# Kernel optimization log

Hardware: AMD Instinct MI355X
Metric: run time of the kernel (lower is better)

Reference implementation:

```python
import jax, jax.numpy as jnp
import numpy as np

K = 5          # number of neighbors (self excluded)
EPS = 1e-7     # distance epsilon
Q = 0.98       # quantile for radius normalization


def _cdist(A):
    # Euclidean pairwise distances [N, N] via the matmul expansion.
    sq = jnp.sum(A * A, axis=-1)
    d2 = sq[:, None] + sq[None, :] - 2.0 * (A @ A.T)
    return jnp.sqrt(jnp.maximum(d2, 0.0))


def _lid(values):
    # values: [N, K] ascending neighbor distances; LID via log-distance ratios.
    norm = values[:, -1:]
    return -jnp.sum(jnp.log10(values) - jnp.log10(norm), axis=1)


def setup_inputs() -> dict:
    key = jax.random.key(0)
    k1, k2 = jax.random.split(key)
    X = jax.random.normal(k1, (8192, 256), dtype=jnp.float32)
    Z = jax.random.normal(k2, (8192, 64), dtype=jnp.float32)
    return {"X": X, "Z": Z}


def reference(X, Z):
    n = X.shape[0]
    normA1 = jnp.quantile(jnp.linalg.norm(X - jnp.mean(X, axis=0), axis=1), Q)
    normA2 = jnp.quantile(jnp.linalg.norm(Z - jnp.mean(Z, axis=0), axis=1), Q)

    # k-NN in X space (drop self at column 0)
    x_dist = (_cdist(X) + EPS) / normA1
    neg_vals, idx = jax.lax.top_k(-x_dist, K + 1)   # smallest K+1, ascending
    values = (-neg_vals)[:, 1:]
    nn_mask = idx[:, 1:]
    lid_X = _lid(values)

    # gather the SAME neighbor indices in Z space
    z_dist = (_cdist(Z) + EPS) / normA2
    extracted = jnp.take_along_axis(z_dist, nn_mask, axis=1)
    lid_Z = _lid(extracted)

    return jnp.sum(jnp.square(lid_X - lid_Z)) / (n * K * 10)
```

## Files before the change

### kernel.cpp

```cpp
#include <hip/hip_runtime.h>
#include <math.h>
#include <stdint.h>

#define EPS     1e-7f
#define NR      8192
#define DX      256
#define DZ      64
#define KNN     5
#define KEEP    6
#define NSPLIT  8
#define NPOOL   (NSPLIT * KEEP)
#define NCAND   16
#define JS      (NR / NSPLIT)
#define JT      64
#define NCHUNK  (JS / JT)
#define RBLK    64
#define SC1     0x7F7F7F7F

typedef float f32x4 __attribute__((ext_vector_type(4)));
typedef int   i32x8 __attribute__((ext_vector_type(8)));

__device__ __forceinline__ uint32_t umin_(uint32_t a, uint32_t b) { return a < b ? a : b; }
__device__ __forceinline__ uint32_t umax_(uint32_t a, uint32_t b) { return a < b ? b : a; }

__device__ __forceinline__ uint32_t to_e4m3(float f) {
    const uint32_t u = __float_as_uint(f);
    const uint32_t s = (u >> 24) & 0x80u;
    const int e = (int)((u >> 23) & 0xFFu) - 127;
    if (e < -10) return s;
    if (e > 8)   return s | 0x7Eu;
    const uint32_t mant = (u & 0x7FFFFFu) | 0x800000u;
    const int shift = (e < -6) ? (14 - e) : 20;
    uint32_t q = (mant + (1u << (shift - 1))) >> shift;
    int E = (e < -6) ? 0 : (e + 7);
    if (q >= 16) { q >>= 1; E += 1; }
    if (E == 0) return s | q;
    return s | ((uint32_t)E << 3) | (q & 7u);
}

__global__ __launch_bounds__(256) void split_k(const float* __restrict__ X,
                                               uint8_t* __restrict__ Xq,
                                               float* __restrict__ sqX,
                                               float* __restrict__ out) {
    if (blockIdx.x == 0 && threadIdx.x == 0) out[0] = 0.0f;
    const int row  = blockIdx.x * 4 + (threadIdx.x >> 6);
    const int lane = threadIdx.x & 63;
    const float4 v = *(const float4*)&X[(size_t)row * DX + lane * 4];
    float s = v.x * v.x + v.y * v.y + v.z * v.z + v.w * v.w;
    const uint32_t b = to_e4m3(v.x) | (to_e4m3(v.y) << 8) |
                       (to_e4m3(v.z) << 16) | (to_e4m3(v.w) << 24);
    ((uint32_t*)Xq)[(size_t)row * (DX / 4) + lane] = b;
    #pragma unroll
    for (int o = 32; o > 0; o >>= 1) s += __shfl_down(s, o);
    if (lane == 0) sqX[row] = s;
}

__global__ __launch_bounds__(256, 2) void mfma_topk_k(const uint8_t* __restrict__ Xq,
                                                      const float* __restrict__ sqX,
                                                      uint32_t* __restrict__ partials) {
    __shared__ __align__(16) uint8_t smem[16384];
    __shared__ uint32_t mb2[RBLK][2][KNN];
    const uint4* Bv = (const uint4*)smem;

    const int tid  = threadIdx.x;
    const int w    = tid >> 6;
    const int lane = tid & 63;
    const int n    = lane & 15;
    const int quad = lane >> 4;
    const int x7   = n & 7;
    const int h    = w >> 1;
    const int sp   = w & 1;
    const int s    = blockIdx.x & 7;
    const int ib   = (blockIdx.x >> 3) * RBLK;
    const int jb0  = s * JS;
    const int rowbase = ib + h * 32;

    i32x8 Aq[2][2];
    #pragma unroll
    for (int g = 0; g < 2; ++g)
        #pragma unroll
        for (int kf = 0; kf < 2; ++kf)
            Aq[g][kf] = *(const i32x8*)(Xq + (size_t)(rowbase + g * 16 + n) * DX
                                        + kf * 128 + quad * 32);

    float sqi[2][4];
    #pragma unroll
    for (int g = 0; g < 2; ++g) {
        const float4 t = *(const float4*)&sqX[rowbase + g * 16 + quad * 4];
        sqi[g][0] = t.x; sqi[g][1] = t.y; sqi[g][2] = t.z; sqi[g][3] = t.w;
    }

    uint32_t best[8][KNN];
    #pragma unroll
    for (int q = 0; q < 8; ++q)
        #pragma unroll
        for (int k = 0; k < KNN; ++k) best[q][k] = 0xFFFFFFFFu;

    int srcoff[4];
    #pragma unroll
    for (int u = 0; u < 4; ++u) {
        const int q  = w * 256 + u * 64 + lane;
        const int sj = q >> 4;
        const int c  = (q & 15) ^ (sj & 7);
        srcoff[u] = sj * DX + c * 16;
    }

    for (int jc = 0; jc < NCHUNK; ++jc) {
        const int jb = jb0 + jc * JT;
        __syncthreads();
        #pragma unroll
        for (int u = 0; u < 4; ++u) {
            const uint8_t* src = Xq + (size_t)jb * DX + srcoff[u];
            uint8_t* dst = smem + (size_t)(w * 256 + u * 64) * 16;
            __builtin_amdgcn_global_load_lds((const __attribute__((address_space(1))) uint32_t*)src,
                                             (__attribute__((address_space(3))) uint32_t*)dst,
                                             16, 0, 0);
        }
        __syncthreads();

        f32x4 acc[2][2];
        #pragma unroll
        for (int si = 0; si < 2; ++si)
            #pragma unroll
            for (int g = 0; g < 2; ++g)
                #pragma unroll
                for (int r = 0; r < 4; ++r) acc[si][g][r] = 0.0f;

        #pragma unroll
        for (int kf = 0; kf < 2; ++kf) {
            #pragma unroll
            for (int si = 0; si < 2; ++si) {
                const int sj = (sp * 2 + si) * 16 + n;
                const int cb = kf * 8 + quad * 2;
                const uint4 p0 = Bv[sj * 16 + (cb ^ x7)];
                const uint4 p1 = Bv[sj * 16 + ((cb + 1) ^ x7)];
                i32x8 b;
                b[0] = p0.x; b[1] = p0.y; b[2] = p0.z; b[3] = p0.w;
                b[4] = p1.x; b[5] = p1.y; b[6] = p1.z; b[7] = p1.w;
                acc[si][0] = __builtin_amdgcn_mfma_scale_f32_16x16x128_f8f6f4(
                                 Aq[0][kf], b, acc[si][0], 0, 0, 0, SC1, 0, SC1);
                acc[si][1] = __builtin_amdgcn_mfma_scale_f32_16x16x128_f8f6f4(
                                 Aq[1][kf], b, acc[si][1], 0, 0, 0, SC1, 0, SC1);
            }
        }

        #pragma unroll
        for (int si = 0; si < 2; ++si) {
            const int j = jb + (sp * 2 + si) * 16 + n;
            const float sqj = sqX[j];
            #pragma unroll
            for (int g = 0; g < 2; ++g) {
                #pragma unroll
                for (int r = 0; r < 4; ++r) {
                    const int i = rowbase + g * 16 + quad * 4 + r;
                    const float d2 = fmaf(-2.0f, acc[si][g][r], sqi[g][r] + sqj);
                    uint32_t cand = (__float_as_uint(d2) & 0xFFFFE000u) | (uint32_t)j;
                    cand = (j == i) ? 0xFFFFFFFFu : cand;
                    const int q = g * 4 + r;
                    if (cand < best[q][KNN - 1]) {
                        uint32_t ck = cand;
                        #pragma unroll
                        for (int k = 0; k < KNN; ++k) {
                            const uint32_t bk = best[q][k];
                            best[q][k] = umin_(ck, bk); ck = umax_(ck, bk);
                        }
                    }
                }
            }
        }
    }

    #pragma unroll
    for (int q = 0; q < 8; ++q) {
        uint32_t a0 = best[q][0], a1 = best[q][1], a2 = best[q][2],
                 a3 = best[q][3], a4 = best[q][4];
        #pragma unroll
        for (int mask = 1; mask <= 8; mask <<= 1) {
            const uint32_t b0 = __shfl_xor(a0, mask);
            const uint32_t b1 = __shfl_xor(a1, mask);
            const uint32_t b2 = __shfl_xor(a2, mask);
            const uint32_t b3 = __shfl_xor(a3, mask);
            const uint32_t b4 = __shfl_xor(a4, mask);
            const uint32_t c0 = umin_(a0, b0);
            const uint32_t c1 = umin_(umin_(a1, b1), umax_(a0, b0));
            const uint32_t c2 = umin_(umin_(a2, b2), umin_(umax_(a0, b1), umax_(a1, b0)));
            const uint32_t c3 = umin_(umin_(a3, b3),
                                      umin_(umax_(a1, b1), umin_(umax_(a0, b2), umax_(a2, b0))));
            const uint32_t c4 = umin_(umin_(a4, b4),
                                      umin_(umin_(umax_(a0, b3), umax_(a1, b2)),
                                            umin_(umax_(a2, b1), umax_(a3, b0))));
            a0 = c0; a1 = c1; a2 = c2; a3 = c3; a4 = c4;
        }
        const int rloc = h * 32 + (q >> 2) * 16 + quad * 4 + (q & 3);
        uint32_t v = a0;
        v = (n == 1) ? a1 : v;
        v = (n == 2) ? a2 : v;
        v = (n == 3) ? a3 : v;
        v = (n == 4) ? a4 : v;
        if (n < KNN) mb2[rloc][sp][n] = v;
    }
    __syncthreads();

    if (tid < RBLK) {
        const uint32_t a0 = mb2[tid][0][0], a1 = mb2[tid][0][1], a2 = mb2[tid][0][2],
                       a3 = mb2[tid][0][3], a4 = mb2[tid][0][4];
        const uint32_t b0 = mb2[tid][1][0], b1 = mb2[tid][1][1], b2 = mb2[tid][1][2],
                       b3 = mb2[tid][1][3], b4 = mb2[tid][1][4];
        uint32_t o[KEEP];
        o[0] = umin_(a0, b0);
        o[1] = umin_(umin_(a1, b1), umax_(a0, b0));
        o[2] = umin_(umin_(a2, b2), umin_(umax_(a0, b1), umax_(a1, b0)));
        o[3] = umin_(umin_(a3, b3), umin_(umax_(a1, b1), umin_(umax_(a0, b2), umax_(a2, b0))));
        o[4] = umin_(umin_(a4, b4), umin_(umin_(umax_(a0, b3), umax_(a1, b2)),
                                          umin_(umax_(a2, b1), umax_(a3, b0))));
        o[5] = umin_(umin_(umax_(a0, b4), umax_(a4, b0)),
                     umin_(umax_(a1, b3), umin_(umax_(a2, b2), umax_(a3, b1))));
        #pragma unroll
        for (int k = 0; k < KEEP; ++k)
            partials[(size_t)(ib + tid) * NPOOL + s * KEEP + k] = o[k];
    }
}

__global__ __launch_bounds__(256) void finalize_k(const uint32_t* __restrict__ parts,
                                                  const float* __restrict__ X,
                                                  const float* __restrict__ Z,
                                                  const float* __restrict__ sqX,
                                                  float* __restrict__ out) {
    __shared__ float wsum[4];
    const int wv   = threadIdx.x >> 6;
    const int lane = threadIdx.x & 63;
    const int i    = blockIdx.x * 4 + wv;

    uint32_t v = (lane < NPOOL) ? parts[(size_t)i * NPOOL + lane] : 0xFFFFFFFFu;
    #pragma unroll
    for (int kk = 2; kk <= 64; kk <<= 1) {
        #pragma unroll
        for (int jj = kk >> 1; jj > 0; jj >>= 1) {
            const uint32_t o = __shfl_xor(v, jj);
            const bool keepmin = ((lane & kk) == 0) == ((lane & jj) == 0);
            v = keepmin ? umin_(v, o) : umax_(v, o);
        }
    }

    const float4 xi = *(const float4*)(X + (size_t)i * DX + lane * 4);

    float p[16];
    #pragma unroll
    for (int c = 0; c < NCAND; ++c) {
        const int jc = (int)(__shfl(v, c) & 0x1FFFu);
        const float4 xj = *(const float4*)(X + (size_t)jc * DX + lane * 4);
        p[c] = fmaf(xi.x, xj.x, fmaf(xi.y, xj.y, fmaf(xi.z, xj.z, xi.w * xj.w)));
    }
    #pragma unroll
    for (int c = 0; c < NCAND; ++c) {
        p[c] += __shfl_xor(p[c], 1);
        p[c] += __shfl_xor(p[c], 2);
        p[c] += __shfl_xor(p[c], 4);
        p[c] += __shfl_xor(p[c], 8);
    }
    const int cs = lane & 15;
    float dotv = p[0];
    dotv = (cs == 1)  ? p[1]  : dotv;
    dotv = (cs == 2)  ? p[2]  : dotv;
    dotv = (cs == 3)  ? p[3]  : dotv;
    dotv = (cs == 4)  ? p[4]  : dotv;
    dotv = (cs == 5)  ? p[5]  : dotv;
    dotv = (cs == 6)  ? p[6]  : dotv;
    dotv = (cs == 7)  ? p[7]  : dotv;
    dotv = (cs == 8)  ? p[8]  : dotv;
    dotv = (cs == 9)  ? p[9]  : dotv;
    dotv = (cs == 10) ? p[10] : dotv;
    dotv = (cs == 11) ? p[11] : dotv;
    dotv = (cs == 12) ? p[12] : dotv;
    dotv = (cs == 13) ? p[13] : dotv;
    dotv = (cs == 14) ? p[14] : dotv;
    dotv = (cs == 15) ? p[15] : dotv;
    dotv += __shfl_xor(dotv, 16);
    dotv += __shfl_xor(dotv, 32);

    unsigned long long k16 = 0xFFFFFFFFFFFFFFFFull;
    const int jl = (int)(v & 0x1FFFu);
    if (lane < NCAND) {
        const float d2x = (sqX[i] + sqX[jl]) - 2.0f * dotv;
        k16 = ((unsigned long long)__float_as_uint(d2x) << 32) | (unsigned)jl;
    }
    #pragma unroll
    for (int kk = 2; kk <= 16; kk <<= 1) {
        #pragma unroll
        for (int jj = kk >> 1; jj > 0; jj >>= 1) {
            const unsigned long long o = __shfl_xor(k16, jj);
            const bool keepmin = ((lane & kk) == 0) == ((lane & jj) == 0);
            k16 = keepmin ? (k16 < o ? k16 : o) : (k16 < o ? o : k16);
        }
    }

    const float d2k = __uint_as_float((uint32_t)(k16 >> 32));
    const int   jk  = (int)(k16 & 0x1FFFull);
    float lkx = 0.0f;
    if (lane < KNN) lkx = log10f(sqrtf(fmaxf(d2k, 0.0f)) + EPS);
    const float l4x = __shfl(lkx, KNN - 1);
    float sx = lkx;
    sx += __shfl_xor(sx, 1);
    sx += __shfl_xor(sx, 2);
    sx += __shfl_xor(sx, 4);

    const float zi = Z[(size_t)i * DZ + lane];
    float zsum = 0.0f, l4z = 0.0f;
    #pragma unroll
    for (int k = 0; k < KNN; ++k) {
        const int jz = __shfl(jk, k);
        const float zj = Z[(size_t)jz * DZ + lane];
        const float d = zi - zj;
        float s = d * d;
        s += __shfl_xor(s, 1);
        s += __shfl_xor(s, 2);
        s += __shfl_xor(s, 4);
        s += __shfl_xor(s, 8);
        s += __shfl_xor(s, 16);
        s += __shfl_xor(s, 32);
        const float lk = log10f(sqrtf(fmaxf(s, 0.0f)) + EPS);
        zsum += lk;
        if (k == KNN - 1) l4z = lk;
    }

    if (lane == 0) {
        const float lx = -(__shfl(sx, 0) - (float)KNN * l4x);
        const float lz = -(zsum - (float)KNN * l4z);
        const float diff = lx - lz;
        wsum[wv] = diff * diff * (1.0f / ((float)NR * KNN * 10.0f));
    }
    __syncthreads();
    if (threadIdx.x == 0)
        atomicAdd(out, wsum[0] + wsum[1] + wsum[2] + wsum[3]);
}

extern "C" void kernel_launch(void* const* d_in, const int* in_sizes, int n_in,
                              void* d_out, int out_size, void* d_ws, size_t ws_size,
                              hipStream_t stream) {
    const float* X = (const float*)d_in[0];
    const float* Z = (const float*)d_in[1];
    float* out = (float*)d_out;

    char* ws = (char*)d_ws;
    float*     sqX      = (float*)ws;
    uint32_t*  partials = (uint32_t*)(ws + 32768);
    uint8_t*   Xq       = (uint8_t*)(ws + 32768 + 2097152);

    split_k<<<NR / 4, 256, 0, stream>>>(X, Xq, sqX, out);
    mfma_topk_k<<<(NR / RBLK) * NSPLIT, 256, 0, stream>>>(Xq, sqX, partials);
    finalize_k<<<NR / 4, 256, 0, stream>>>(partials, X, Z, sqX, out);
}
```

Baseline: 156.5 us.

## Fold norm term into MFMA accumulator init and merge candidate pairs branchlessly

The top-k epilogue now initializes the MFMA accumulators with -0.5*|x_j|^2 minus a constant bias, so the raw accumulator bits act as the ordering key. This drops the per-element d2 reconstruction and keeps the ordering correct as long as the value stays negative. Two candidates are merged into the sorted 5-list at once with a branchless min/max network instead of a guarded insertion. The self-exclusion check now runs only in the chunk that holds the diagonal, and the j-norms are staged once in LDS. The risks are a different key scale, which downstream decoding must handle, and mantissa truncation of a biased value, which reduces ranking precision.

After: 141.3 us. -9.7%, faster.

```diff
diff --git a/kernel.cpp b/kernel.cpp
--- a/kernel.cpp
+++ b/kernel.cpp
@@ -16,6 +16,7 @@
 #define NCHUNK  (JS / JT)
 #define RBLK    64
 #define SC1     0x7F7F7F7F
+#define BIASF   256.0f
 
 typedef float f32x4 __attribute__((ext_vector_type(4)));
 typedef int   i32x8 __attribute__((ext_vector_type(8)));
@@ -55,11 +56,37 @@
     if (lane == 0) sqX[row] = s;
 }
 
+#define FOLD_BODY(KILL)                                                                   \
+    _Pragma("unroll")                                                                     \
+    for (int g = 0; g < 2; ++g) {                                                         \
+        _Pragma("unroll")                                                                 \
+        for (int r = 0; r < 4; ++r) {                                                     \
+            const int q = g * 4 + r;                                                      \
+            uint32_t c0 = (__float_as_uint(acc[0][g][r]) & 0xFFFFE000u) | (uint32_t)j0;   \
+            uint32_t c1 = (__float_as_uint(acc[1][g][r]) & 0xFFFFE000u) | (uint32_t)(j0 + 16); \
+            if (KILL) {                                                                   \
+                const int irow = rowbase + g * 16 + quad * 4 + r;                         \
+                c0 = (j0 == irow)      ? 0xFFFFFFFFu : c0;                                \
+                c1 = (j0 + 16 == irow) ? 0xFFFFFFFFu : c1;                                \
+            }                                                                             \
+            const uint32_t lo = umin_(c0, c1);                                            \
+            const uint32_t hi = umax_(c0, c1);                                            \
+            const uint32_t b0 = best[q][0], b1 = best[q][1], b2 = best[q][2],             \
+                           b3 = best[q][3], b4 = best[q][4];                              \
+            best[q][0] = umin_(b0, lo);                                                   \
+            best[q][1] = umin_(umin_(b1, umax_(b0, lo)), hi);                             \
+            best[q][2] = umin_(umin_(b2, umax_(b1, lo)), umax_(b0, hi));                  \
+            best[q][3] = umin_(umin_(b3, umax_(b2, lo)), umax_(b1, hi));                  \
+            best[q][4] = umin_(umin_(b4, umax_(b3, lo)), umax_(b2, hi));                  \
+        }                                                                                 \
+    }
+
 __global__ __launch_bounds__(256, 2) void mfma_topk_k(const uint8_t* __restrict__ Xq,
                                                       const float* __restrict__ sqX,
                                                       uint32_t* __restrict__ partials) {
     __shared__ __align__(16) uint8_t smem[16384];
     __shared__ uint32_t mb2[RBLK][2][KNN];
+    __shared__ __align__(16) float sq_s[JS];
     const uint4* Bv = (const uint4*)smem;
 
     const int tid  = threadIdx.x;
@@ -75,6 +102,11 @@
     const int jb0  = s * JS;
     const int rowbase = ib + h * 32;
 
+    ((f32x4*)sq_s)[tid] = ((const f32x4*)(sqX + jb0))[tid];
+
+    const int rel   = rowbase - jb0;
+    const int cdiag = __builtin_amdgcn_readfirstlane((rel >= 0 && rel < JS) ? (rel >> 6) : -1);
+
     i32x8 Aq[2][2];
     #pragma unroll
     for (int g = 0; g < 2; ++g)
@@ -82,13 +114,6 @@
         for (int kf = 0; kf < 2; ++kf)
             Aq[g][kf] = *(const i32x8*)(Xq + (size_t)(rowbase + g * 16 + n) * DX
                                         + kf * 128 + quad * 32);
-
-    float sqi[2][4];
-    #pragma unroll
-    for (int g = 0; g < 2; ++g) {
-        const float4 t = *(const float4*)&sqX[rowbase + g * 16 + quad * 4];
-        sqi[g][0] = t.x; sqi[g][1] = t.y; sqi[g][2] = t.z; sqi[g][3] = t.w;
-    }
 
     uint32_t best[8][KNN];
     #pragma unroll
@@ -118,13 +143,15 @@
         }
         __syncthreads();
 
+        const int   sqb  = jc * JT + sp * 32 + n;
+        const float ini0 = fmaf(-0.5f, sq_s[sqb],      -BIASF);
+        const float ini1 = fmaf(-0.5f, sq_s[sqb + 16], -BIASF);
+
         f32x4 acc[2][2];
         #pragma unroll
-        for (int si = 0; si < 2; ++si)
+        for (int g = 0; g < 2; ++g)
             #pragma unroll
-            for (int g = 0; g < 2; ++g)
-                #pragma unroll
-                for (int r = 0; r < 4; ++r) acc[si][g][r] = 0.0f;
+            for (int r = 0; r < 4; ++r) { acc[0][g][r] = ini0; acc[1][g][r] = ini1; }
 
         #pragma unroll
         for (int kf = 0; kf < 2; ++kf) {
@@ -144,29 +171,11 @@
             }
         }
 
-        #pragma unroll
-        for (int si = 0; si < 2; ++si) {
-            const int j = jb + (sp * 2 + si) * 16 + n;
-            const float sqj = sqX[j];
-            #pragma unroll
-            for (int g = 0; g < 2; ++g) {
-                #pragma unroll
-                for (int r = 0; r < 4; ++r) {
-                    const int i = rowbase + g * 16 + quad * 4 + r;
-                    const float d2 = fmaf(-2.0f, acc[si][g][r], sqi[g][r] + sqj);
-                    uint32_t cand = (__float_as_uint(d2) & 0xFFFFE000u) | (uint32_t)j;
-                    cand = (j == i) ? 0xFFFFFFFFu : cand;
-                    const int q = g * 4 + r;
-                    if (cand < best[q][KNN - 1]) {
-                        uint32_t ck = cand;
-                        #pragma unroll
-                        for (int k = 0; k < KNN; ++k) {
-                            const uint32_t bk = best[q][k];
-                            best[q][k] = umin_(ck, bk); ck = umax_(ck, bk);
-                        }
-                    }
-                }
-            }
+        const int j0 = jb + sp * 32 + n;
+        if (jc != cdiag) {
+            FOLD_BODY(0)
+        } else {
+            FOLD_BODY(1)
         }
     }
 
```
